# Kernel tuning notes

Hardware: AMD Instinct MI355X
Metric: run time of the kernel (lower is better)

Reference implementation:

```python
import jax, jax.numpy as jnp
import numpy as np

U, N, L, C, D, B = 50000, 50000, 10, 256, 64, 4096


def setup_inputs() -> dict:
    key = jax.random.key(0)
    ks = jax.random.split(key, 12)
    xav = float(np.sqrt(6.0 / (D + D)))  # xavier_uniform bound for [D, D]
    return {
        "items": jax.random.randint(ks[0], (U, L), 0, N),
        "time_embs": jax.random.normal(ks[1], (U, L, D), dtype=jnp.float32),
        "user_embedding": jax.random.normal(ks[2], (U, D), dtype=jnp.float32),
        "item_embedding": jax.random.normal(ks[3], (N, D), dtype=jnp.float32),
        "cluster_emb": jax.random.normal(ks[4], (C, D), dtype=jnp.float32),
        "w_filters": jax.random.normal(ks[5], (U, L, D), dtype=jnp.float32),
        "Wq": jax.random.uniform(ks[6], (D, D), jnp.float32, -xav, xav),
        "Wk": jax.random.uniform(ks[7], (D, D), jnp.float32, -xav, xav),
        "Wv": jax.random.uniform(ks[8], (D, D), jnp.float32, -xav, xav),
        "users": jax.random.randint(ks[9], (B,), 0, U),
        "pos_items": jax.random.randint(ks[10], (B,), 0, N),
        "neg_items": jax.random.randint(ks[11], (B,), 0, N),
        "alpha1": jnp.float32(1.0),
        "alpha2": jnp.float32(1.0),
        "alpha3": jnp.float32(1.0),
    }


def reference(items, time_embs, user_embedding, item_embedding, cluster_emb,
              w_filters, Wq, Wk, Wv, users, pos_items, neg_items,
              alpha1, alpha2, alpha3):
    d = Wq.shape[0]
    # short_items_embs built under torch.no_grad / .detach() in the original
    short = jax.lax.stop_gradient(
        user_embedding[:, None, :] + item_embedding[items] + time_embs)  # [U,L,D]
    Q = short @ Wq                                   # [U,L,D]
    K = cluster_emb @ Wk                             # [C,D]
    V = cluster_emb @ Wv                             # [C,D]
    scores = jnp.einsum("uld,cd->ulc", Q, K) / jnp.sqrt(jnp.float32(d))
    attn = jax.nn.softmax(scores, axis=-1)           # [U,L,C]
    shorted = jnp.einsum("ulc,cd->uld", attn, V)     # [U,L,D]
    # matrix_filter = shorted^T @ w_filter per user -> [U,D,D]
    mfilt = jnp.einsum("uld,ule->ude", shorted, w_filters)
    new_user = jnp.einsum("ud,ude->ue", user_embedding, mfilt)  # [U,D]
    mix = alpha3 * (alpha1 * user_embedding + alpha2 * new_user)
    u_g = mix[users]                     # [B,D]
    pos_g = item_embedding[pos_items]    # [B,D]
    neg_g = item_embedding[neg_items]    # [B,D]
    return (u_g, pos_g, neg_g)
```

## Files before the change

kernel.cpp:

```cpp
#include <hip/hip_runtime.h>

#define D 64
#define L 10
#define C 256
#define G 4
#define SWB 72

typedef __attribute__((ext_vector_type(8))) short bf16x8;
typedef __attribute__((ext_vector_type(4))) short short4v;
typedef __attribute__((ext_vector_type(4))) float f32x4;

__device__ inline short f2bf(float f) {
  unsigned u = __float_as_uint(f);
  u = (u + 0x7FFFu + ((u >> 16) & 1u)) >> 16;
  return (short)u;
}
__device__ inline float4 add3(float4 a, float4 b, float4 c) {
  return make_float4(a.x + b.x + c.x, a.y + b.y + c.y, a.z + b.z + c.z, a.w + b.w + c.w);
}
__device__ inline short4v f2bf4(float4 a) {
  short4v r;
  r[0] = f2bf(a.x); r[1] = f2bf(a.y); r[2] = f2bf(a.z); r[3] = f2bf(a.w);
  return r;
}

__global__ __launch_bounds__(256) void pre(const float* __restrict__ cl,
                                           const float* __restrict__ Wk,
                                           const float* __restrict__ Wq,
                                           const float* __restrict__ Wv,
                                           short* __restrict__ Bf) {
  __shared__ float s_cl[4 * 64];
  __shared__ float s_kc[4 * 64];
  __shared__ float s_w[64 * 65];
  const int t = threadIdx.x;
  const int bh = blockIdx.x >> 6, cb = blockIdx.x & 63;
  const int c0 = cb * 4;
  const int r = t >> 6, j = t & 63;

  s_cl[t] = cl[c0 * 64 + t];
  if (bh == 0) {
#pragma unroll
    for (int i = 0; i < 4; ++i) {
      int e = i * 256 + t;
      float4 v = ((const float4*)Wq)[e];
      int k = e >> 4, q = e & 15;
      float* dst = &s_w[k * 65 + q * 4];
      dst[0] = v.x; dst[1] = v.y; dst[2] = v.z; dst[3] = v.w;
    }
  }
  __syncthreads();

  const float* __restrict__ Wx = bh ? Wv : Wk;
  float acc = 0.f;
#pragma unroll 8
  for (int m = 0; m < 64; ++m) acc += s_cl[r * 64 + m] * Wx[m * 64 + j];

  if (bh == 1) {
    Bf[(c0 + r) * 128 + 64 + j] = f2bf(acc);
    return;
  }
  s_kc[t] = acc;
  __syncthreads();

  float o = 0.f;
#pragma unroll 8
  for (int jj = 0; jj < 64; ++jj) o += s_kc[r * 64 + jj] * s_w[j * 65 + jj];
  Bf[(c0 + r) * 128 + j] = f2bf(0.125f * o);
}

__global__ __launch_bounds__(256, 4) void filter_main(
    const int* __restrict__ items, const float* __restrict__ te,
    const float* __restrict__ ue_g, const float* __restrict__ ie_g,
    const float* __restrict__ wf_g, const short* __restrict__ Bf,
    const int* __restrict__ users, const int* __restrict__ pos_items,
    const int* __restrict__ neg_items, const float* __restrict__ a1p,
    const float* __restrict__ a2p, const float* __restrict__ a3p,
    float* __restrict__ out, int B) {
  __shared__ short s_shb[40 * SWB];
  __shared__ short s_ueb[G * SWB];
  __shared__ float2 s_red[G][12][4];

  const int tid = threadIdx.x, w = tid >> 6, lane = tid & 63;
  const int col16 = lane & 15, kb = lane >> 4;
  const int qr = col16 >> 2, jr = col16 & 3;
  const int b4 = blockIdx.x * G;
  const int BD = B * D;

  const int us0 = users[b4], us1 = users[b4 + 1];
  const int us2 = users[b4 + 2], us3 = users[b4 + 3];
  const int usw = (w == 0) ? us0 : ((w == 1) ? us1 : ((w == 2) ? us2 : us3));

  const float uev = ue_g[usw * D + lane];
  const float posv = ie_g[pos_items[b4 + w] * D + lane];
  const float negv = ie_g[neg_items[b4 + w] * D + lane];
  float wfv[L];
#pragma unroll
  for (int l = 0; l < L; ++l) wfv[l] = wf_g[(usw * L + l) * D + lane];
  const float a1 = *a1p, a2 = *a2p, a3 = *a3p;

  s_ueb[w * SWB + lane] = f2bf(uev);

  {
    const float4* te4 = (const float4*)te;
    const float4* ie4 = (const float4*)ie_g;
    const float4* ue4 = (const float4*)ue_g;
    const int grp = tid >> 4, j = tid & 15;
#pragma unroll
    for (int it = 0; it < 3; ++it) {
      int row = it * 16 + grp;
      if (row < 40) {
        int g = row / 10, l = row - g * 10;
        int uu = (g == 0) ? us0 : ((g == 1) ? us1 : ((g == 2) ? us2 : us3));
        int itm = items[uu * L + l];
        float4 t = te4[(uu * L + l) * 16 + j];
        float4 e = ie4[itm * 16 + j];
        float4 uf = ue4[uu * 16 + j];
        *(short4v*)&s_shb[row * SWB + j * 4] = f2bf4(add3(t, e, uf));
      }
    }
  }
  __syncthreads();

  bf16x8 a00, a01, a10, a11, a20, a21, au0 = {}, au1 = {};
#define FRAG(AV0, AV1, MT)                                                     \
  {                                                                            \
    int p = (MT)*4 + jr;                                                       \
    int g = p / 3;                                                             \
    int l = (p - g * 3) * 4 + qr;                                              \
    if (l < L) {                                                               \
      const bf16x8* rp = (const bf16x8*)&s_shb[(g * 10 + l) * SWB];            \
      AV0 = rp[kb];                                                            \
      AV1 = rp[4 + kb];                                                        \
    } else {                                                                   \
      AV0 = bf16x8{};                                                          \
      AV1 = bf16x8{};                                                          \
    }                                                                          \
  }
  FRAG(a00, a01, 0)
  FRAG(a10, a11, 1)
  FRAG(a20, a21, 2)
  if (col16 < G) {
    const bf16x8* rp = (const bf16x8*)&s_ueb[col16 * SWB];
    au0 = rp[kb];
    au1 = rp[4 + kb];
  }

  float Sa[3][4], Ta[3][4];
#pragma unroll
  for (int mt = 0; mt < 3; ++mt)
#pragma unroll
    for (int jj = 0; jj < 4; ++jj) { Sa[mt][jj] = 0.f; Ta[mt][jj] = 0.f; }

#pragma unroll
  for (int nt = 0; nt < 4; ++nt) {
    const bf16x8* bp = (const bf16x8*)(Bf + ((w * 4 + nt) * 16 + col16) * 128);
    bf16x8 b0 = bp[kb], b1 = bp[4 + kb], b2 = bp[8 + kb], b3 = bp[12 + kb];
    f32x4 z = {0.f, 0.f, 0.f, 0.f};
    f32x4 c0 = z, c1 = z, c2 = z, cu = z;
    c0 = __builtin_amdgcn_mfma_f32_16x16x32_bf16(a00, b0, c0, 0, 0, 0);
    c0 = __builtin_amdgcn_mfma_f32_16x16x32_bf16(a01, b1, c0, 0, 0, 0);
    c1 = __builtin_amdgcn_mfma_f32_16x16x32_bf16(a10, b0, c1, 0, 0, 0);
    c1 = __builtin_amdgcn_mfma_f32_16x16x32_bf16(a11, b1, c1, 0, 0, 0);
    c2 = __builtin_amdgcn_mfma_f32_16x16x32_bf16(a20, b0, c2, 0, 0, 0);
    c2 = __builtin_amdgcn_mfma_f32_16x16x32_bf16(a21, b1, c2, 0, 0, 0);
    cu = __builtin_amdgcn_mfma_f32_16x16x32_bf16(au0, b2, cu, 0, 0, 0);
    cu = __builtin_amdgcn_mfma_f32_16x16x32_bf16(au1, b3, cu, 0, 0, 0);
    float vu0 = __shfl(cu[0], col16, 64);
    float vu1 = __shfl(cu[1], col16, 64);
    float vu2 = __shfl(cu[2], col16, 64);
    float vu3 = __shfl(cu[3], col16, 64);
#pragma unroll
    for (int mt = 0; mt < 3; ++mt)
#pragma unroll
      for (int jj = 0; jj < 4; ++jj) {
        float sv = (mt == 0) ? c0[jj] : (mt == 1) ? c1[jj] : c2[jj];
        float e = __expf(sv);
        const int g = (mt * 4 + jj) / 3;
        float vu = (g == 0) ? vu0 : ((g == 1) ? vu1 : ((g == 2) ? vu2 : vu3));
        Sa[mt][jj] += e;
        Ta[mt][jj] += e * vu;
      }
  }

#pragma unroll
  for (int mt = 0; mt < 3; ++mt)
#pragma unroll
    for (int jj = 0; jj < 4; ++jj) {
      float S = Sa[mt][jj], T = Ta[mt][jj];
      S += __shfl_xor(S, 1, 64); T += __shfl_xor(T, 1, 64);
      S += __shfl_xor(S, 2, 64); T += __shfl_xor(T, 2, 64);
      S += __shfl_xor(S, 4, 64); T += __shfl_xor(T, 4, 64);
      S += __shfl_xor(S, 8, 64); T += __shfl_xor(T, 8, 64);
      if (col16 == 0) {
        const int g = (mt * 4 + jj) / 3, sub = (mt * 4 + jj) % 3;
        s_red[g][sub * 4 + kb][w] = make_float2(S, T);
      }
    }
  __syncthreads();

  float nu = 0.f;
#pragma unroll
  for (int l = 0; l < L; ++l) {
    float2 p0 = s_red[w][l][0], p1 = s_red[w][l][1];
    float2 p2 = s_red[w][l][2], p3 = s_red[w][l][3];
    float S = (p0.x + p1.x) + (p2.x + p3.x);
    float T = (p0.y + p1.y) + (p2.y + p3.y);
    nu += T * __frcp_rn(S) * wfv[l];
  }
  out[(b4 + w) * D + lane] = a3 * (a1 * uev + a2 * nu);
  out[BD + (b4 + w) * D + lane] = posv;
  out[2 * BD + (b4 + w) * D + lane] = negv;
}

extern "C" void kernel_launch(void* const* d_in, const int* in_sizes, int n_in,
                              void* d_out, int out_size, void* d_ws, size_t ws_size,
                              hipStream_t stream) {
  const int* items = (const int*)d_in[0];
  const float* time_embs = (const float*)d_in[1];
  const float* user_emb = (const float*)d_in[2];
  const float* item_emb = (const float*)d_in[3];
  const float* cluster = (const float*)d_in[4];
  const float* wf = (const float*)d_in[5];
  const float* Wq = (const float*)d_in[6];
  const float* Wk = (const float*)d_in[7];
  const float* Wv = (const float*)d_in[8];
  const int* users = (const int*)d_in[9];
  const int* pos = (const int*)d_in[10];
  const int* neg = (const int*)d_in[11];
  const float* a1 = (const float*)d_in[12];
  const float* a2 = (const float*)d_in[13];
  const float* a3 = (const float*)d_in[14];
  const int B = in_sizes[9];

  short* Bf = (short*)d_ws;
  hipLaunchKernelGGL(pre, dim3(128), dim3(256), 0, stream,
                     cluster, Wk, Wq, Wv, Bf);
  hipLaunchKernelGGL(filter_main, dim3(B / G), dim3(256), 0, stream,
                     items, time_embs, user_emb, item_emb, wf, Bf,
                     users, pos, neg, a1, a2, a3, (float*)d_out, B);
}
```

Before: 29.00 us.

## Move gather/staging of short embeddings into the precompute kernel via workspace

The random gathers of time, item and user embeddings, their sum and bf16 conversion now run in the first kernel, in extra blocks alongside the K/V precompute. The results go to a workspace buffer that the MFMA kernel then reads with contiguous vector loads. The pos/neg item copies also move into the first kernel. This takes the latency-bound gathers off the GEMM kernel's critical path and overlaps them with the precompute, at the cost of an extra global write and read of the staged rows.

Result: slower. 30.28 us (+4.4%).

```diff
diff --git a/kernel.cpp b/kernel.cpp
--- a/kernel.cpp
+++ b/kernel.cpp
@@ -5,6 +5,9 @@
 #define C 256
 #define G 4
 #define SWB 72
+#define NROWS 44
+#define STAGE_ROWS 52
+#define PRE_BLOCKS 128
 
 typedef __attribute__((ext_vector_type(8))) short bf16x8;
 typedef __attribute__((ext_vector_type(4))) short short4v;
@@ -24,99 +27,112 @@
   return r;
 }
 
-__global__ __launch_bounds__(256) void pre(const float* __restrict__ cl,
-                                           const float* __restrict__ Wk,
-                                           const float* __restrict__ Wq,
-                                           const float* __restrict__ Wv,
-                                           short* __restrict__ Bf) {
+__global__ __launch_bounds__(256) void stage_pre(
+    const float* __restrict__ cl, const float* __restrict__ Wk,
+    const float* __restrict__ Wq, const float* __restrict__ Wv,
+    const int* __restrict__ items, const float* __restrict__ te,
+    const float* __restrict__ ue_g, const float* __restrict__ ie_g,
+    const int* __restrict__ users, const int* __restrict__ pos_items,
+    const int* __restrict__ neg_items, short* __restrict__ Bf,
+    short* __restrict__ wsrows, float* __restrict__ out, int B, int NUG) {
   __shared__ float s_cl[4 * 64];
   __shared__ float s_kc[4 * 64];
   __shared__ float s_w[64 * 65];
   const int t = threadIdx.x;
-  const int bh = blockIdx.x >> 6, cb = blockIdx.x & 63;
-  const int c0 = cb * 4;
-  const int r = t >> 6, j = t & 63;
-
-  s_cl[t] = cl[c0 * 64 + t];
-  if (bh == 0) {
-#pragma unroll
-    for (int i = 0; i < 4; ++i) {
-      int e = i * 256 + t;
-      float4 v = ((const float4*)Wq)[e];
-      int k = e >> 4, q = e & 15;
-      float* dst = &s_w[k * 65 + q * 4];
-      dst[0] = v.x; dst[1] = v.y; dst[2] = v.z; dst[3] = v.w;
-    }
-  }
-  __syncthreads();
-
-  const float* __restrict__ Wx = bh ? Wv : Wk;
-  float acc = 0.f;
+
+  if (blockIdx.x < PRE_BLOCKS) {
+    const int bh = blockIdx.x >> 6, cb = blockIdx.x & 63;
+    const int c0 = cb * 4;
+    const int r = t >> 6, j = t & 63;
+    s_cl[t] = cl[c0 * 64 + t];
+    if (bh == 0) {
+#pragma unroll
+      for (int i = 0; i < 4; ++i) {
+        int e = i * 256 + t;
+        float4 v = ((const float4*)Wq)[e];
+        int k = e >> 4, q = e & 15;
+        float* dst = &s_w[k * 65 + q * 4];
+        dst[0] = v.x; dst[1] = v.y; dst[2] = v.z; dst[3] = v.w;
+      }
+    }
+    __syncthreads();
+    const float* __restrict__ Wx = bh ? Wv : Wk;
+    float acc = 0.f;
 #pragma unroll 8
-  for (int m = 0; m < 64; ++m) acc += s_cl[r * 64 + m] * Wx[m * 64 + j];
-
-  if (bh == 1) {
-    Bf[(c0 + r) * 128 + 64 + j] = f2bf(acc);
+    for (int m = 0; m < 64; ++m) acc += s_cl[r * 64 + m] * Wx[m * 64 + j];
+    if (bh == 1) {
+      Bf[(c0 + r) * 128 + 64 + j] = f2bf(acc);
+      return;
+    }
+    s_kc[t] = acc;
+    __syncthreads();
+    float o = 0.f;
+#pragma unroll 8
+    for (int jj = 0; jj < 64; ++jj) o += s_kc[r * 64 + jj] * s_w[j * 65 + jj];
+    Bf[(c0 + r) * 128 + j] = f2bf(0.125f * o);
     return;
   }
-  s_kc[t] = acc;
-  __syncthreads();
-
-  float o = 0.f;
-#pragma unroll 8
-  for (int jj = 0; jj < 64; ++jj) o += s_kc[r * 64 + jj] * s_w[j * 65 + jj];
-  Bf[(c0 + r) * 128 + j] = f2bf(0.125f * o);
-}
-
-__global__ __launch_bounds__(256, 4) void filter_main(
-    const int* __restrict__ items, const float* __restrict__ te,
-    const float* __restrict__ ue_g, const float* __restrict__ ie_g,
-    const float* __restrict__ wf_g, const short* __restrict__ Bf,
-    const int* __restrict__ users, const int* __restrict__ pos_items,
-    const int* __restrict__ neg_items, const float* __restrict__ a1p,
+
+  const int sb = blockIdx.x - PRE_BLOCKS;
+  const int rid = sb * 16 + (t >> 4);
+  const int j = t & 15;
+  const int ug = rid / STAGE_ROWS;
+  const int r = rid - ug * STAGE_ROWS;
+  if (ug >= NUG) return;
+  const float4* te4 = (const float4*)te;
+  const float4* ie4 = (const float4*)ie_g;
+  const float4* ue4 = (const float4*)ue_g;
+  const int BD = B * D;
+
+  if (r < 40) {
+    int g = r / 10, l = r - g * 10;
+    int u = users[ug * G + g];
+    int itm = items[u * L + l];
+    float4 v = add3(te4[(u * L + l) * 16 + j], ie4[itm * 16 + j], ue4[u * 16 + j]);
+    *(short4v*)&wsrows[(ug * NROWS + r) * 64 + j * 4] = f2bf4(v);
+  } else if (r < 44) {
+    int g = r - 40;
+    int u = users[ug * G + g];
+    *(short4v*)&wsrows[(ug * NROWS + 40 + g) * 64 + j * 4] = f2bf4(ue4[u * 16 + j]);
+  } else if (r < 48) {
+    int g = r - 44, row = ug * G + g;
+    *(float4*)&out[BD + row * D + j * 4] = ie4[pos_items[row] * 16 + j];
+  } else {
+    int g = r - 48, row = ug * G + g;
+    *(float4*)&out[2 * BD + row * D + j * 4] = ie4[neg_items[row] * 16 + j];
+  }
+}
+
+__global__ __launch_bounds__(256, 4) void gemm_main(
+    const short* __restrict__ wsrows, const short* __restrict__ Bf,
+    const float* __restrict__ ue_g, const float* __restrict__ wf_g,
+    const int* __restrict__ users, const float* __restrict__ a1p,
     const float* __restrict__ a2p, const float* __restrict__ a3p,
     float* __restrict__ out, int B) {
-  __shared__ short s_shb[40 * SWB];
-  __shared__ short s_ueb[G * SWB];
+  __shared__ short s_shb[NROWS * SWB];
   __shared__ float2 s_red[G][12][4];
 
   const int tid = threadIdx.x, w = tid >> 6, lane = tid & 63;
   const int col16 = lane & 15, kb = lane >> 4;
   const int qr = col16 >> 2, jr = col16 & 3;
   const int b4 = blockIdx.x * G;
-  const int BD = B * D;
-
-  const int us0 = users[b4], us1 = users[b4 + 1];
-  const int us2 = users[b4 + 2], us3 = users[b4 + 3];
-  const int usw = (w == 0) ? us0 : ((w == 1) ? us1 : ((w == 2) ? us2 : us3));
-
+
+  const int usw = users[b4 + w];
   const float uev = ue_g[usw * D + lane];
-  const float posv = ie_g[pos_items[b4 + w] * D + lane];
-  const float negv = ie_g[neg_items[b4 + w] * D + lane];
   float wfv[L];
 #pragma unroll
   for (int l = 0; l < L; ++l) wfv[l] = wf_g[(usw * L + l) * D + lane];
   const float a1 = *a1p, a2 = *a2p, a3 = *a3p;
 
-  s_ueb[w * SWB + lane] = f2bf(uev);
-
   {
-    const float4* te4 = (const float4*)te;
-    const float4* ie4 = (const float4*)ie_g;
-    const float4* ue4 = (const float4*)ue_g;
-    const int grp = tid >> 4, j = tid & 15;
-#pragma unroll
-    for (int it = 0; it < 3; ++it) {
-      int row = it * 16 + grp;
-      if (row < 40) {
-        int g = row / 10, l = row - g * 10;
-        int uu = (g == 0) ? us0 : ((g == 1) ? us1 : ((g == 2) ? us2 : us3));
-        int itm = items[uu * L + l];
-        float4 t = te4[(uu * L + l) * 16 + j];
-        float4 e = ie4[itm * 16 + j];
-        float4 uf = ue4[uu * 16 + j];
-        *(short4v*)&s_shb[row * SWB + j * 4] = f2bf4(add3(t, e, uf));
-      }
+    const int base = blockIdx.x * NROWS * 64;
+#pragma unroll
+    for (int pass = 0; pass < 2; ++pass) {
+      int idx = pass * 256 + tid;
+      int row = idx >> 3, ch = idx & 7;
+      if (row < NROWS)
+        *(bf16x8*)&s_shb[row * SWB + ch * 8] =
+            *(const bf16x8*)&wsrows[base + row * 64 + ch * 8];
     }
   }
   __syncthreads();
@@ -140,7 +156,7 @@
   FRAG(a10, a11, 1)
   FRAG(a20, a21, 2)
   if (col16 < G) {
-    const bf16x8* rp = (const bf16x8*)&s_ueb[col16 * SWB];
+    const bf16x8* rp = (const bf16x8*)&s_shb[(40 + col16) * SWB];
     au0 = rp[kb];
     au1 = rp[4 + kb];
   }
@@ -208,8 +224,6 @@
     nu += T * __frcp_rn(S) * wfv[l];
   }
   out[(b4 + w) * D + lane] = a3 * (a1 * uev + a2 * nu);
-  out[BD + (b4 + w) * D + lane] = posv;
-  out[2 * BD + (b4 + w) * D + lane] = negv;
 }
 
 extern "C" void kernel_launch(void* const* d_in, const int* in_sizes, int n_in,
@@ -231,11 +245,15 @@
   const float* a2 = (const float*)d_in[13];
   const float* a3 = (const float*)d_in[14];
   const int B = in_sizes[9];
+  const int NUG = B / G;
 
   short* Bf = (short*)d_ws;
-  hipLaunchKernelGGL(pre, dim3(128), dim3(256), 0, stream,
-                     cluster, Wk, Wq, Wv, Bf);
-  hipLaunchKernelGGL(filter_main, dim3(B / G), dim3(256), 0, stream,
-                     items, time_embs, user_emb, item_emb, wf, Bf,
-                     users, pos, neg, a1, a2, a3, (float*)d_out, B);
-}
+  short* wsrows = Bf + C * 128;
+  const int stage_blocks = (NUG * STAGE_ROWS + 15) / 16;
+  hipLaunchKernelGGL(stage_pre, dim3(PRE_BLOCKS + stage_blocks), dim3(256), 0,
+                     stream, cluster, Wk, Wq, Wv, items, time_embs, user_emb,
+                     item_emb, users, pos, neg, Bf, wsrows, (float*)d_out, B, NUG);
+  hipLaunchKernelGGL(gemm_main, dim3(NUG), dim3(256), 0, stream,
+                     wsrows, Bf, user_emb, wf, users, a1, a2, a3,
+                     (float*)d_out, B);
+}
```
